# Performance work log

Measured on AMD Instinct MI355X. Metric: run time of the kernel, lower is better.

Reference implementation:

```python
import jax, jax.numpy as jnp
import numpy as np

EMBED_DIM = 1152
NUM_HEADS = 16
HEAD_DIM = EMBED_DIM // NUM_HEADS  # 72
SCALE = HEAD_DIM ** -0.5


def setup_inputs() -> dict:
    key = jax.random.key(0)
    ks = jax.random.split(key, 5)
    B, S, D = 32, 729, EMBED_DIM
    hidden_states = jax.random.normal(ks[0], (B, S, D), dtype=jnp.float32)
    # fused QKV projection weight/bias (q|k|v concatenated on output dim)
    w_qkv = jax.random.normal(ks[1], (D, 3 * D), dtype=jnp.float32) * (D ** -0.5)
    b_qkv = jax.random.normal(ks[2], (3 * D,), dtype=jnp.float32) * 0.02
    w_out = jax.random.normal(ks[3], (D, D), dtype=jnp.float32) * (D ** -0.5)
    b_out = jax.random.normal(ks[4], (D,), dtype=jnp.float32) * 0.02
    return {"hidden_states": hidden_states, "w_qkv": w_qkv, "b_qkv": b_qkv,
            "w_out": w_out, "b_out": b_out}


def reference(hidden_states, w_qkv, b_qkv, w_out, b_out):
    B, S, D = hidden_states.shape
    qkv = hidden_states @ w_qkv + b_qkv              # [B,S,3D]
    q, k, v = jnp.split(qkv, 3, axis=-1)
    # [B,S,D] -> [B,H,S,hd]
    def to_heads(x):
        return x.reshape(B, S, NUM_HEADS, HEAD_DIM).transpose(0, 2, 1, 3)
    q, k, v = to_heads(q), to_heads(k), to_heads(v)
    scores = jnp.einsum('bhqd,bhkd->bhqk', q, k) * SCALE
    attn = jax.nn.softmax(scores, axis=-1)
    out = jnp.einsum('bhqk,bhkd->bhqd', attn, v)     # [B,H,S,hd]
    out = out.transpose(0, 2, 1, 3).reshape(B, S, D)
    return out @ w_out + b_out
```

## Files before the change

kernel.cpp:

```cpp
#include <hip/hip_runtime.h>
#include <hip/hip_bf16.h>
#include <stdint.h>

typedef unsigned short u16;
typedef __attribute__((ext_vector_type(8))) short bf16x8;
typedef __attribute__((ext_vector_type(4))) float f32x4;
typedef __attribute__((ext_vector_type(4))) unsigned short us4;

#define T_TOK   23328
#define MPAD    23424
#define DMODEL  1152
#define N3      3456
#define NHEAD   16
#define HDIM    72
#define SEQ     729
#define VSTR    736
#define SCALE_F 0.1178511301977579f
#define KVB     64
#define NT      12
#define THR     8.0f

__device__ __forceinline__ u16 f2bf(float f) {
  unsigned u = __builtin_bit_cast(unsigned, f);
  u += 0x7fffu + ((u >> 16) & 1u);
  return (u16)(u >> 16);
}

__device__ __forceinline__ f32x4 mfma16(bf16x8 a, bf16x8 b, f32x4 c) {
  return __builtin_amdgcn_mfma_f32_16x16x32_bf16(a, b, c, 0, 0, 0);
}

#define GL16(g, l)                                                        \
  __builtin_amdgcn_global_load_lds(                                       \
      (const __attribute__((address_space(1))) void*)(g),                 \
      (__attribute__((address_space(3))) void*)(l), 16, 0, 0)


__global__ void k_cvt_hidden(const float* __restrict__ in, u16* __restrict__ out) {
  size_t i4 = ((size_t)blockIdx.x * blockDim.x + threadIdx.x) * 4;
  if (i4 >= (size_t)MPAD * DMODEL) return;
  us4 o;
  if (i4 < (size_t)T_TOK * DMODEL) {
    float4 v = *(const float4*)(in + i4);
    o[0] = f2bf(v.x); o[1] = f2bf(v.y); o[2] = f2bf(v.z); o[3] = f2bf(v.w);
  } else {
    o[0] = 0; o[1] = 0; o[2] = 0; o[3] = 0;
  }
  *(us4*)(out + i4) = o;
}

template <int R, int C>
__global__ void k_transpose(const float* __restrict__ w, u16* __restrict__ wt) {
  size_t i = (size_t)blockIdx.x * blockDim.x + threadIdx.x;
  if (i >= (size_t)R * C) return;
  int n  = (int)(i / R);
  int kk = (int)(i - (size_t)n * R);
  wt[i] = f2bf(w[(size_t)kk * C + n]);
}

template <int EPI>
__global__ __launch_bounds__(256) void k_gemm(
    const u16* __restrict__ A, const u16* __restrict__ Bt,
    const float* __restrict__ bias,
    u16* __restrict__ qo, u16* __restrict__ ko, u16* __restrict__ vTo,
    float* __restrict__ outp)
{
  __shared__ u16 As[128 * 32];
  __shared__ u16 Bs[128 * 32];
  const int tid  = threadIdx.x;
  const int wave = tid >> 6;
  const int lane = tid & 63;
  const int m0 = blockIdx.y * 128;
  const int n0 = blockIdx.x * 128;
  const int wm = (wave >> 1) * 64;
  const int wn = (wave & 1) * 64;

  const int rofs = wave * 16 + (lane >> 2);
  const int cofs = (lane & 3) * 8;
  const u16* gA0 = A  + (size_t)(m0 + rofs) * DMODEL + cofs;
  const u16* gA1 = gA0 + (size_t)64 * DMODEL;
  const u16* gB0 = Bt + (size_t)(n0 + rofs) * DMODEL + cofs;
  const u16* gB1 = gB0 + (size_t)64 * DMODEL;
  char* lA0 = (char*)As + wave * 1024;
  char* lA1 = (char*)As + 4096 + wave * 1024;
  char* lB0 = (char*)Bs + wave * 1024;
  char* lB1 = (char*)Bs + 4096 + wave * 1024;

  const int fr = lane & 15;
  const int fk = (lane >> 4) * 8;

  f32x4 acc[4][4] = {};

  for (int kt = 0; kt < DMODEL; kt += 32) {
    GL16(gA0 + kt, lA0);
    GL16(gA1 + kt, lA1);
    GL16(gB0 + kt, lB0);
    GL16(gB1 + kt, lB1);
    __syncthreads();
    bf16x8 af[4], bfrag[4];
#pragma unroll
    for (int i = 0; i < 4; ++i)
      af[i] = *(const bf16x8*)&As[(wm + i * 16 + fr) * 32 + fk];
#pragma unroll
    for (int j = 0; j < 4; ++j)
      bfrag[j] = *(const bf16x8*)&Bs[(wn + j * 16 + fr) * 32 + fk];
#pragma unroll
    for (int i = 0; i < 4; ++i)
#pragma unroll
      for (int j = 0; j < 4; ++j)
        acc[i][j] = mfma16(af[i], bfrag[j], acc[i][j]);
    __syncthreads();
  }

#pragma unroll
  for (int j = 0; j < 4; ++j) {
    const int n = n0 + wn + j * 16 + fr;
    const float bi = bias[n];
    if (EPI == 0) {
      const int which = n / DMODEL;
      const int rr = n - which * DMODEL;
      const int h = rr / HDIM;
      const int d = rr - h * HDIM;
#pragma unroll
      for (int i = 0; i < 4; ++i) {
        const int tr = m0 + wm + i * 16 + (lane >> 4) * 4;
#pragma unroll
        for (int rg = 0; rg < 4; ++rg) {
          const int t = tr + rg;
          if (t < T_TOK) {
            const int bb = t / SEQ;
            const int s  = t - bb * SEQ;
            const int bh = bb * NHEAD + h;
            const float val = acc[i][j][rg] + bi;
            if (which == 0)
              qo[((size_t)bh * SEQ + s) * HDIM + d] = f2bf(val * SCALE_F);
            else if (which == 1)
              ko[((size_t)bh * SEQ + s) * HDIM + d] = f2bf(val);
            else
              vTo[((size_t)bh * HDIM + d) * VSTR + s] = f2bf(val);
          }
        }
      }
    } else {
#pragma unroll
      for (int i = 0; i < 4; ++i) {
        const int tr = m0 + wm + i * 16 + (lane >> 4) * 4;
#pragma unroll
        for (int rg = 0; rg < 4; ++rg) {
          const int t = tr + rg;
          if (t < T_TOK)
            outp[(size_t)t * DMODEL + n] = acc[i][j][rg] + bi;
        }
      }
    }
  }
}


__device__ __forceinline__ void stage_kv(const u16* __restrict__ kb, const u16* __restrict__ vb,
                                         u16* KsB, u16* VsB, int kt, int wv, int lane) {
#pragma unroll
  for (int rdi = 0; rdi < 2; ++rdi) {
    const int c0 = rdi * 256 + wv * 64;
    {
      const int c = c0 + lane;
      const int row = c / 9;
      const int off = (c - row * 9) * 8;
      GL16(kb + (size_t)(kt + row) * HDIM + off, KsB + (size_t)c0 * 8);
    }
    {
      const int c = c0 + lane;
      const int d = c >> 3;
      int off = kt + (((c & 7) ^ (d & 7)) << 3);
      off = off > (VSTR - 8) ? (VSTR - 8) : off;
      GL16(vb + (size_t)d * VSTR + off, VsB + (size_t)c0 * 8);
    }
  }
  if (wv == 0) {
    const int c = 512 + lane;
    const int row = c / 9;
    const int off = (c - row * 9) * 8;
    GL16(kb + (size_t)(kt + row) * HDIM + off, KsB + (size_t)512 * 8);
    const int d = c >> 3;
    int voff = kt + (((c & 7) ^ (d & 7)) << 3);
    voff = voff > (VSTR - 8) ? (VSTR - 8) : voff;
    GL16(vb + (size_t)d * VSTR + voff, VsB + (size_t)512 * 8);
  }
}

__global__ __launch_bounds__(256) void k_attn(
    const u16* __restrict__ q, const u16* __restrict__ k,
    const u16* __restrict__ vT, u16* __restrict__ aout)
{
  __shared__ alignas(16) u16 Ks[2][4640];
  __shared__ alignas(16) u16 Vs[2][5120];
  __shared__ alignas(16) u16 pl[4][16][72];

  const int tid  = threadIdx.x;
  const int wv   = tid >> 6;
  const int lane = tid & 63;
  const int fr = lane & 15;
  const int fg = lane >> 4;
  const int fk = fg * 8;

  const int bh = blockIdx.y;
  const int qbase = blockIdx.x * 64 + wv * 16;

  const u16* qb = q  + (size_t)bh * (SEQ * HDIM);
  const u16* kb = k  + (size_t)bh * (SEQ * HDIM);
  const u16* vb = vT + (size_t)bh * (HDIM * VSTR);

  if (tid < 64) { Vs[0][4608 + tid] = 0x3F80; Vs[1][4608 + tid] = 0x3F80; }
  for (int i = tid; i < 448; i += 256) { Vs[0][4672 + i] = 0; Vs[1][4672 + i] = 0; }
  if (tid < 32) { Ks[0][4608 + tid] = 0; Ks[1][4608 + tid] = 0; }

  const int qrow = qbase + fr;
  bf16x8 qf0 = {}, qf1 = {}, qf2 = {};
  if (qrow < SEQ) {
    const u16* qp = qb + (size_t)qrow * HDIM;
    qf0 = *(const bf16x8*)(qp + fk);
    qf1 = *(const bf16x8*)(qp + 32 + fk);
    if (fg == 0) qf2 = *(const bf16x8*)(qp + 64);
  }

  f32x4 oacc[5] = {};
  float mrun[4] = {-1e30f, -1e30f, -1e30f, -1e30f};

  stage_kv(kb, vb, Ks[0], Vs[0], 0, wv, lane);
  __syncthreads();

  int buf = 0;
  for (int t = 0; t < NT; ++t) {
    const int kt = t * KVB;
    if (t + 1 < NT)
      stage_kv(kb, vb, Ks[buf ^ 1], Vs[buf ^ 1], kt + KVB, wv, lane);

    const char* kB = (const char*)Ks[buf];
    f32x4 sc[4];
#pragma unroll
    for (int hh = 0; hh < 4; ++hh) {
      const char* krow = kB + (hh * 16 + fr) * 144;
      bf16x8 kf0 = *(const bf16x8*)(krow + fg * 16);
      bf16x8 kf1 = *(const bf16x8*)(krow + 64 + fg * 16);
      bf16x8 kf2 = *(const bf16x8*)(krow + 128 + fg * 16);
      f32x4 z = {};
      z = mfma16(qf0, kf0, z);
      z = mfma16(qf1, kf1, z);
      z = mfma16(qf2, kf2, z);
      sc[hh] = z;
    }
    if (kt + KVB > SEQ) {
#pragma unroll
      for (int hh = 0; hh < 4; ++hh)
        if (kt + hh * 16 + fr >= SEQ) {
          sc[hh][0] = -1e30f; sc[hh][1] = -1e30f; sc[hh][2] = -1e30f; sc[hh][3] = -1e30f;
        }
    }

    float tmx[4];
    bool needs = false;
#pragma unroll
    for (int r = 0; r < 4; ++r) {
      tmx[r] = fmaxf(fmaxf(sc[0][r], sc[1][r]), fmaxf(sc[2][r], sc[3][r]));
      needs |= (tmx[r] > mrun[r] + THR);
    }
    if (__any(needs)) {
#pragma unroll
      for (int r = 0; r < 4; ++r) {
        float tm = tmx[r];
        tm = fmaxf(tm, __shfl_xor(tm, 1));
        tm = fmaxf(tm, __shfl_xor(tm, 2));
        tm = fmaxf(tm, __shfl_xor(tm, 4));
        tm = fmaxf(tm, __shfl_xor(tm, 8));
        const float mnew = fmaxf(mrun[r], tm);
        const float resc = __expf(mrun[r] - mnew);
        mrun[r] = mnew;
#pragma unroll
        for (int v = 0; v < 5; ++v) oacc[v][r] *= resc;
      }
    }
#pragma unroll
    for (int r = 0; r < 4; ++r) {
      const int prow = fg * 4 + r;
#pragma unroll
      for (int hh = 0; hh < 4; ++hh)
        pl[wv][prow][hh * 16 + fr] = f2bf(__expf(sc[hh][r] - mrun[r]));
    }

    const bf16x8 pa0 = *(const bf16x8*)&pl[wv][fr][fk];
    const bf16x8 pa1 = *(const bf16x8*)&pl[wv][fr][32 + fk];
    const char* vB = (const char*)Vs[buf];
    const int swz = (fr & 7) << 4;
#pragma unroll
    for (int v = 0; v < 5; ++v) {
      const char* vrow = vB + (size_t)(v * 16 + fr) * 128;
      bf16x8 vf0 = *(const bf16x8*)(vrow + ((fg * 16) ^ swz));
      bf16x8 vf1 = *(const bf16x8*)(vrow + (((4 + fg) * 16) ^ swz));
      oacc[v] = mfma16(pa0, vf0, oacc[v]);
      oacc[v] = mfma16(pa1, vf1, oacc[v]);
    }

    __syncthreads();
    buf ^= 1;
  }

  const int bb = bh >> 4, h = bh & 15;
#pragma unroll
  for (int r = 0; r < 4; ++r) {
    const int row = qbase + fg * 4 + r;
    if (row < SEQ) {
      const float l = __shfl(oacc[4][r], (lane & 48) | 8);
      const float inv = 1.0f / l;
      u16* op = aout + (size_t)(bb * SEQ + row) * DMODEL + h * HDIM;
#pragma unroll
      for (int v = 0; v < 5; ++v) {
        const int d = v * 16 + fr;
        if (d < HDIM) op[d] = f2bf(oacc[v][r] * inv);
      }
    }
  }
}

extern "C" void kernel_launch(void* const* d_in, const int* in_sizes, int n_in,
                              void* d_out, int out_size, void* d_ws, size_t ws_size,
                              hipStream_t stream) {
  (void)in_sizes; (void)n_in; (void)out_size; (void)ws_size;
  const float* hs   = (const float*)d_in[0];
  const float* wqkv = (const float*)d_in[1];
  const float* bqkv = (const float*)d_in[2];
  const float* wout = (const float*)d_in[3];
  const float* bout = (const float*)d_in[4];
  float* out = (float*)d_out;

  u16* hbuf  = (u16*)d_ws;
  u16* wqkvT = hbuf  + (size_t)MPAD * DMODEL;
  u16* woutT = wqkvT + (size_t)N3 * DMODEL;
  u16* qb    = woutT + (size_t)DMODEL * DMODEL;
  u16* kb    = qb    + (size_t)512 * SEQ * HDIM;
  u16* vTb   = kb    + (size_t)512 * SEQ * HDIM;

  k_cvt_hidden<<<(MPAD * DMODEL / 4 + 255) / 256, 256, 0, stream>>>(hs, hbuf);
  k_transpose<DMODEL, N3><<<((size_t)DMODEL * N3 + 255) / 256, 256, 0, stream>>>(wqkv, wqkvT);
  k_transpose<DMODEL, DMODEL><<<((size_t)DMODEL * DMODEL + 255) / 256, 256, 0, stream>>>(wout, woutT);
  k_gemm<0><<<dim3(N3 / 128, MPAD / 128), 256, 0, stream>>>(hbuf, wqkvT, bqkv, qb, kb, vTb, nullptr);
  k_attn<<<dim3(12, 512), 256, 0, stream>>>(qb, kb, vTb, hbuf);
  k_gemm<1><<<dim3(DMODEL / 128, MPAD / 128), 256, 0, stream>>>(hbuf, woutT, bout,
                                                                nullptr, nullptr, nullptr, out);
}
```

Before: 882.9 us.

## Double-buffer GEMM LDS tiles and remap workgroups for XCD locality

The bf16 GEMM kernels now load the next K-slice into a second LDS buffer while computing on the current one, which removes one barrier per iteration and overlaps global loads with MFMA work. The 2D grid is flattened to 1D, and block IDs are remapped so that consecutive tiles land on the same XCD, aiming to improve L2 reuse of A and B tiles. LDS use per block doubles, which can lower occupancy. The stage for the next buffer is issued before the current buffer is read, so correctness depends on the barrier at the end of each iteration.

Result: slower. 956.3 us (+8.3%).

```diff
diff --git a/kernel.cpp b/kernel.cpp
--- a/kernel.cpp
+++ b/kernel.cpp
@@ -58,20 +58,27 @@
   wt[i] = f2bf(w[(size_t)kk * C + n]);
 }
 
-template <int EPI>
+template <int EPI, int GX>
 __global__ __launch_bounds__(256) void k_gemm(
     const u16* __restrict__ A, const u16* __restrict__ Bt,
     const float* __restrict__ bias,
     u16* __restrict__ qo, u16* __restrict__ ko, u16* __restrict__ vTo,
     float* __restrict__ outp)
 {
-  __shared__ u16 As[128 * 32];
-  __shared__ u16 Bs[128 * 32];
+  __shared__ u16 As[2][4096];
+  __shared__ u16 Bs[2][4096];
   const int tid  = threadIdx.x;
   const int wave = tid >> 6;
   const int lane = tid & 63;
-  const int m0 = blockIdx.y * 128;
-  const int n0 = blockIdx.x * 128;
+
+  constexpr int nwg = GX * 183;
+  constexpr int q8 = nwg >> 3, r8 = nwg & 7;
+  const int bid = blockIdx.x;
+  const int xcd = bid & 7, idx = bid >> 3;
+  const int wgid = (xcd < r8 ? xcd * (q8 + 1) : r8 * (q8 + 1) + (xcd - r8) * q8) + idx;
+  const int m0 = (wgid / GX) * 128;
+  const int n0 = (wgid % GX) * 128;
+
   const int wm = (wave >> 1) * 64;
   const int wn = (wave & 1) * 64;
 
@@ -81,35 +88,42 @@
   const u16* gA1 = gA0 + (size_t)64 * DMODEL;
   const u16* gB0 = Bt + (size_t)(n0 + rofs) * DMODEL + cofs;
   const u16* gB1 = gB0 + (size_t)64 * DMODEL;
-  char* lA0 = (char*)As + wave * 1024;
-  char* lA1 = (char*)As + 4096 + wave * 1024;
-  char* lB0 = (char*)Bs + wave * 1024;
-  char* lB1 = (char*)Bs + 4096 + wave * 1024;
 
   const int fr = lane & 15;
   const int fk = (lane >> 4) * 8;
 
+  auto stage = [&](int kt, int b) {
+    char* a_ = (char*)As + b * 8192 + wave * 1024;
+    char* b_ = (char*)Bs + b * 8192 + wave * 1024;
+    GL16(gA0 + kt, a_);
+    GL16(gA1 + kt, a_ + 4096);
+    GL16(gB0 + kt, b_);
+    GL16(gB1 + kt, b_ + 4096);
+  };
+
   f32x4 acc[4][4] = {};
 
+  stage(0, 0);
+  __syncthreads();
+
+  int buf = 0;
   for (int kt = 0; kt < DMODEL; kt += 32) {
-    GL16(gA0 + kt, lA0);
-    GL16(gA1 + kt, lA1);
-    GL16(gB0 + kt, lB0);
-    GL16(gB1 + kt, lB1);
-    __syncthreads();
+    if (kt + 32 < DMODEL)
+      stage(kt + 32, buf ^ 1);
     bf16x8 af[4], bfrag[4];
 #pragma unroll
     for (int i = 0; i < 4; ++i)
-      af[i] = *(const bf16x8*)&As[(wm + i * 16 + fr) * 32 + fk];
+      af[i] = *(const bf16x8*)&As[buf][(wm + i * 16 + fr) * 32 + fk];
 #pragma unroll
     for (int j = 0; j < 4; ++j)
-      bfrag[j] = *(const bf16x8*)&Bs[(wn + j * 16 + fr) * 32 + fk];
+      bfrag[j] = *(const bf16x8*)&Bs[buf][(wn + j * 16 + fr) * 32 + fk];
 #pragma unroll
     for (int i = 0; i < 4; ++i)
 #pragma unroll
       for (int j = 0; j < 4; ++j)
         acc[i][j] = mfma16(af[i], bfrag[j], acc[i][j]);
     __syncthreads();
+    buf ^= 1;
   }
 
 #pragma unroll
@@ -342,8 +356,7 @@
   k_cvt_hidden<<<(MPAD * DMODEL / 4 + 255) / 256, 256, 0, stream>>>(hs, hbuf);
   k_transpose<DMODEL, N3><<<((size_t)DMODEL * N3 + 255) / 256, 256, 0, stream>>>(wqkv, wqkvT);
   k_transpose<DMODEL, DMODEL><<<((size_t)DMODEL * DMODEL + 255) / 256, 256, 0, stream>>>(wout, woutT);
-  k_gemm<0><<<dim3(N3 / 128, MPAD / 128), 256, 0, stream>>>(hbuf, wqkvT, bqkv, qb, kb, vTb, nullptr);
+  k_gemm<0, 27><<<27 * 183, 256, 0, stream>>>(hbuf, wqkvT, bqkv, qb, kb, vTb, nullptr);
   k_attn<<<dim3(12, 512), 256, 0, stream>>>(qb, kb, vTb, hbuf);
-  k_gemm<1><<<dim3(DMODEL / 128, MPAD / 128), 256, 0, stream>>>(hbuf, woutT, bout,
-                                                                nullptr, nullptr, nullptr, out);
-}
+  k_gemm<1, 9><<<9 * 183, 256, 0, stream>>>(hbuf, woutT, bout, nullptr, nullptr, nullptr, out);
+}
```
